# Kernel optimization log

Measured on AMD Instinct MI355X. Metric: run time of the kernel, lower is better.

The kernel has to match this reference:

```python
import jax, jax.numpy as jnp
import numpy as np

ALPHA = 0.2  # LeakyReLU negative slope
NEG_BIG = -9e15

def setup_inputs() -> dict:
    key = jax.random.key(0)
    k1, k2, k3, k4 = jax.random.split(key, 4)
    N, F_in, F_out = 8192, 512, 64
    inp = jax.random.normal(k1, (N, F_in), dtype=jnp.float32)
    adj = jax.random.randint(k2, (N, N), 0, 2, dtype=jnp.int32)
    W = jax.random.normal(k3, (F_in, F_out), dtype=jnp.float32) * (1.414 / np.sqrt(F_in + F_out))
    a = jax.random.normal(k4, (2 * F_out, 1), dtype=jnp.float32) * 0.1
    return {"input": inp, "adj": adj, "W": W, "a": a}

def reference(input, adj, W, a):
    # h: [N, F_out]
    h = input @ W
    F_out = h.shape[1]
    # Decompose a into a1 (source part) and a2 (target part):
    a1 = a[:F_out, 0]   # [F_out]
    a2 = a[F_out:, 0]   # [F_out]
    s1 = h @ a1         # [N]
    s2 = h @ a2         # [N]
    e = s1[:, None] + s2[None, :]                      # [N, N]
    e = jnp.where(e > 0, e, ALPHA * e)                 # LeakyReLU
    e = jnp.where(adj > 0, e, jnp.float32(NEG_BIG))    # mask non-edges
    attention = jax.nn.softmax(e, axis=1)              # [N, N]
    # dropout with p=0.0 / eval mode -> identity
    h_prime = attention @ h                            # [N, F_out]
    return h_prime
```

## Files before the change

kernel.cpp:

```cpp
#include <hip/hip_runtime.h>
#include <hip/hip_bf16.h>

constexpr int N    = 8192;
constexpr int FIN  = 512;
constexpr int FOUT = 64;
constexpr int NSPLIT = 32;
constexpr int JCHUNK = N / NSPLIT;
constexpr int LROW   = JCHUNK + 8;

typedef __attribute__((ext_vector_type(8))) short short8;
typedef __attribute__((ext_vector_type(4))) float f32x4;

__global__ __launch_bounds__(256) void k1_proj(
    const float* __restrict__ input, const float* __restrict__ W,
    const float* __restrict__ a, __hip_bfloat16* __restrict__ hbT,
    float* __restrict__ E1, float* __restrict__ F1,
    float* __restrict__ E2, float* __restrict__ F2)
{
    __shared__ __hip_bfloat16 tile[8][64];
    const int tid  = threadIdx.x;
    const int col  = tid & 63;
    const int g    = tid >> 6;
    const int rbase = blockIdx.x * 8;

    float acc[2] = {0.f, 0.f};
    const float* in0 = input + (size_t)(rbase + g * 2) * FIN;

    for (int k = 0; k < FIN; k += 8) {
        float w[8];
        #pragma unroll
        for (int q = 0; q < 8; ++q) w[q] = W[(k + q) * FOUT + col];
        const float4 x0a = *(const float4*)(in0 + 0 * FIN + k);
        const float4 x0b = *(const float4*)(in0 + 0 * FIN + k + 4);
        const float4 x1a = *(const float4*)(in0 + 1 * FIN + k);
        const float4 x1b = *(const float4*)(in0 + 1 * FIN + k + 4);
        acc[0] = fmaf(x0a.w, w[3], fmaf(x0a.z, w[2], fmaf(x0a.y, w[1], fmaf(x0a.x, w[0], acc[0]))));
        acc[0] = fmaf(x0b.w, w[7], fmaf(x0b.z, w[6], fmaf(x0b.y, w[5], fmaf(x0b.x, w[4], acc[0]))));
        acc[1] = fmaf(x1a.w, w[3], fmaf(x1a.z, w[2], fmaf(x1a.y, w[1], fmaf(x1a.x, w[0], acc[1]))));
        acc[1] = fmaf(x1b.w, w[7], fmaf(x1b.z, w[6], fmaf(x1b.y, w[5], fmaf(x1b.x, w[4], acc[1]))));
    }

    const float a1c = a[col];
    const float a2c = a[FOUT + col];
    #pragma unroll
    for (int q = 0; q < 2; ++q) {
        float r1 = acc[q] * a1c;
        float r2 = acc[q] * a2c;
        #pragma unroll
        for (int off = 32; off >= 1; off >>= 1) {
            r1 += __shfl_xor(r1, off, 64);
            r2 += __shfl_xor(r2, off, 64);
        }
        if (col == 0) {
            const int i = rbase + g * 2 + q;
            E1[i] = __expf(r1);
            F1[i] = __expf(0.2f * r1);
            E2[i] = __expf(r2);
            F2[i] = __expf(0.2f * r2);
        }
        tile[g * 2 + q][col] = __float2bfloat16(acc[q]);
    }
    __syncthreads();

    if (tid < 128) {
        const int c = tid >> 1, part = tid & 1;
        unsigned short v[4];
        #pragma unroll
        for (int u = 0; u < 4; ++u) {
            __hip_bfloat16 hv = tile[part * 4 + u][c];
            v[u] = *reinterpret_cast<unsigned short*>(&hv);
        }
        *(ushort4*)((unsigned short*)hbT + (size_t)c * N + rbase + part * 4) =
            make_ushort4(v[0], v[1], v[2], v[3]);
    }
}

__global__ __launch_bounds__(256, 4) void k2_attn(
    const int* __restrict__ adj,
    const float* __restrict__ E1, const float* __restrict__ F1,
    const float* __restrict__ E2, const float* __restrict__ F2,
    const unsigned short* __restrict__ hbT,
    float* __restrict__ pAcc, float* __restrict__ pZ)
{
    __shared__ unsigned short Bl[64 * LROW];
    __shared__ unsigned int   Ml[64 * 9];
    __shared__ float          E2l[JCHUNK];
    __shared__ float          F2l[JCHUNK];

    const int r   = blockIdx.x;
    const int s   = blockIdx.y;
    const int tid = threadIdx.x;
    const int w     = tid >> 6;
    const int lane  = tid & 63;
    const int row16 = lane & 15;
    const int quad  = lane >> 4;
    const int jbeg  = s * JCHUNK;

    #pragma unroll
    for (int rr = 0; rr < 8; ++rr) {
        const int seg = rr * 256 + tid;
        const int f = seg >> 5, o = seg & 31;
        const short8 v = *(const short8*)((const short*)hbT + (size_t)f * N + jbeg + o * 8);
        *(short8*)(&Bl[f * LROW + o * 8]) = v;
    }
    {
        unsigned char* Mlb = (unsigned char*)Ml;
        #pragma unroll
        for (int it = 0; it < 16; ++it) {
            const int rloc = it * 4 + w;
            const int4 av = *(const int4*)(adj + (size_t)(r * 64 + rloc) * N + jbeg + lane * 4);
            unsigned int nib =
                (av.x != 0 ? 1u : 0u) | (av.y != 0 ? 2u : 0u) |
                (av.z != 0 ? 4u : 0u) | (av.w != 0 ? 8u : 0u);
            const unsigned int other = __shfl_xor(nib, 1, 64);
            if (!(lane & 1))
                Mlb[rloc * 36 + (lane >> 1)] = (unsigned char)(nib | (other << 4));
        }
    }
    E2l[tid] = E2[jbeg + tid];
    F2l[tid] = F2[jbeg + tid];
    __syncthreads();

    const int iloc = w * 16 + row16;
    const int i    = r * 64 + iloc;
    const float E1i = E1[i];
    const float F1i = F1[i];

    f32x4 acc0 = {0.f, 0.f, 0.f, 0.f};
    f32x4 acc1 = {0.f, 0.f, 0.f, 0.f};
    f32x4 acc2 = {0.f, 0.f, 0.f, 0.f};
    f32x4 acc3 = {0.f, 0.f, 0.f, 0.f};
    float zpart = 0.f;

    #pragma unroll
    for (int it = 0; it < JCHUNK / 32; ++it) {
        const int jj = it * 32 + quad * 8;

        const unsigned int mword = Ml[iloc * 9 + it];
        const unsigned int mbyte = (mword >> (8 * quad)) & 0xffu;

        const float4 eA = *(const float4*)(&E2l[jj]);
        const float4 eB = *(const float4*)(&E2l[jj + 4]);
        const float4 fA = *(const float4*)(&F2l[jj]);
        const float4 fB = *(const float4*)(&F2l[jj + 4]);

        const short8 b0 = *(const short8*)(&Bl[(row16 +  0) * LROW + jj]);
        const short8 b1 = *(const short8*)(&Bl[(row16 + 16) * LROW + jj]);
        const short8 b2 = *(const short8*)(&Bl[(row16 + 32) * LROW + jj]);
        const short8 b3 = *(const short8*)(&Bl[(row16 + 48) * LROW + jj]);

        float e2v[8], f2v[8];
        e2v[0] = eA.x; e2v[1] = eA.y; e2v[2] = eA.z; e2v[3] = eA.w;
        e2v[4] = eB.x; e2v[5] = eB.y; e2v[6] = eB.z; e2v[7] = eB.w;
        f2v[0] = fA.x; f2v[1] = fA.y; f2v[2] = fA.z; f2v[3] = fA.w;
        f2v[4] = fB.x; f2v[5] = fB.y; f2v[6] = fB.z; f2v[7] = fB.w;

        short8 afrag;
        #pragma unroll
        for (int j = 0; j < 8; ++j) {
            float pv = fmaxf(E1i * e2v[j], F1i * f2v[j]);
            pv = ((mbyte >> j) & 1u) ? pv : 0.f;
            __hip_bfloat16 hv = __float2bfloat16(pv);
            zpart += __bfloat162float(hv);
            afrag[j] = *reinterpret_cast<short*>(&hv);
        }

        acc0 = __builtin_amdgcn_mfma_f32_16x16x32_bf16(afrag, b0, acc0, 0, 0, 0);
        acc1 = __builtin_amdgcn_mfma_f32_16x16x32_bf16(afrag, b1, acc1, 0, 0, 0);
        acc2 = __builtin_amdgcn_mfma_f32_16x16x32_bf16(afrag, b2, acc2, 0, 0, 0);
        acc3 = __builtin_amdgcn_mfma_f32_16x16x32_bf16(afrag, b3, acc3, 0, 0, 0);
    }

    zpart += __shfl_xor(zpart, 16, 64);
    zpart += __shfl_xor(zpart, 32, 64);
    if (quad == 0) pZ[(size_t)s * N + i] = zpart;

    float* outp = pAcc + ((size_t)s * N + (size_t)r * 64 + w * 16) * FOUT;
    #pragma unroll
    for (int reg = 0; reg < 4; ++reg) {
        const int row = quad * 4 + reg;
        outp[row * FOUT + ( 0 + row16)] = acc0[reg];
        outp[row * FOUT + (16 + row16)] = acc1[reg];
        outp[row * FOUT + (32 + row16)] = acc2[reg];
        outp[row * FOUT + (48 + row16)] = acc3[reg];
    }
}

__global__ __launch_bounds__(256) void k3_combine(
    const float* __restrict__ pAcc, const float* __restrict__ pZ,
    float* __restrict__ out)
{
    const int idx = blockIdx.x * 256 + threadIdx.x;
    const int i = idx >> 6;
    float num = 0.f, den = 0.f;
    #pragma unroll
    for (int s = 0; s < NSPLIT; ++s) {
        num += pAcc[(size_t)s * N * FOUT + idx];
        den += pZ[(size_t)s * N + i];
    }
    out[idx] = num / den;
}

extern "C" void kernel_launch(void* const* d_in, const int* in_sizes, int n_in,
                              void* d_out, int out_size, void* d_ws, size_t ws_size,
                              hipStream_t stream)
{
    const float* input = (const float*)d_in[0];
    const int*   adj   = (const int*)d_in[1];
    const float* W     = (const float*)d_in[2];
    const float* a     = (const float*)d_in[3];
    float* out = (float*)d_out;

    char* ws = (char*)d_ws;
    __hip_bfloat16* hbT = (__hip_bfloat16*)ws;
    float* E1   = (float*)(ws + (size_t)FOUT * N * 2);
    float* F1   = E1 + N;
    float* E2   = F1 + N;
    float* F2   = E2 + N;
    float* pZ   = F2 + N;
    float* pAcc = pZ + (size_t)NSPLIT * N;

    k1_proj<<<N / 8, 256, 0, stream>>>(input, W, a, hbT, E1, F1, E2, F2);

    dim3 g2(N / 64, NSPLIT);
    k2_attn<<<g2, 256, 0, stream>>>(adj, E1, F1, E2, F2,
                                    (const unsigned short*)hbT, pAcc, pZ);

    k3_combine<<<(N * FOUT) / 256, 256, 0, stream>>>(pAcc, pZ, out);
}
```

Measured before the change: 451.9 us.

## Reduce split-K partials by looping slices per block and compute row sums via MFMA

Lowers the number of j-splits from 32 to 8. Each block now walks four 256-column slices of its chunk in sequence, so the pAcc/pZ partial buffers and the combine kernel read a quarter of the data. The row-sum denominator is now computed by an extra MFMA against a ones vector instead of scalar adds plus shuffles. It also uses a packed bf16x2 conversion. In exchange the grid is 4x smaller (1024 blocks), and each slice's loads are serialized behind barriers with no overlap.

```diff
diff --git a/kernel.cpp b/kernel.cpp
--- a/kernel.cpp
+++ b/kernel.cpp
@@ -4,12 +4,16 @@
 constexpr int N    = 8192;
 constexpr int FIN  = 512;
 constexpr int FOUT = 64;
-constexpr int NSPLIT = 32;
+constexpr int NSPLIT = 8;
 constexpr int JCHUNK = N / NSPLIT;
-constexpr int LROW   = JCHUNK + 8;
+constexpr int NSLICE = 4;
+constexpr int JS     = JCHUNK / NSLICE;
+constexpr int LROW   = JS + 8;
 
 typedef __attribute__((ext_vector_type(8))) short short8;
 typedef __attribute__((ext_vector_type(4))) float f32x4;
+
+union BF2U { unsigned int u; __hip_bfloat162 h; };
 
 __global__ __launch_bounds__(256) void k1_proj(
     const float* __restrict__ input, const float* __restrict__ W,
@@ -84,8 +88,8 @@
 {
     __shared__ unsigned short Bl[64 * LROW];
     __shared__ unsigned int   Ml[64 * 9];
-    __shared__ float          E2l[JCHUNK];
-    __shared__ float          F2l[JCHUNK];
+    __shared__ float          E2l[JS];
+    __shared__ float          F2l[JS];
 
     const int r   = blockIdx.x;
     const int s   = blockIdx.y;
@@ -94,86 +98,103 @@
     const int lane  = tid & 63;
     const int row16 = lane & 15;
     const int quad  = lane >> 4;
-    const int jbeg  = s * JCHUNK;
-
-    #pragma unroll
-    for (int rr = 0; rr < 8; ++rr) {
-        const int seg = rr * 256 + tid;
-        const int f = seg >> 5, o = seg & 31;
-        const short8 v = *(const short8*)((const short*)hbT + (size_t)f * N + jbeg + o * 8);
-        *(short8*)(&Bl[f * LROW + o * 8]) = v;
-    }
-    {
-        unsigned char* Mlb = (unsigned char*)Ml;
-        #pragma unroll
-        for (int it = 0; it < 16; ++it) {
-            const int rloc = it * 4 + w;
-            const int4 av = *(const int4*)(adj + (size_t)(r * 64 + rloc) * N + jbeg + lane * 4);
-            unsigned int nib =
-                (av.x != 0 ? 1u : 0u) | (av.y != 0 ? 2u : 0u) |
-                (av.z != 0 ? 4u : 0u) | (av.w != 0 ? 8u : 0u);
-            const unsigned int other = __shfl_xor(nib, 1, 64);
-            if (!(lane & 1))
-                Mlb[rloc * 36 + (lane >> 1)] = (unsigned char)(nib | (other << 4));
-        }
-    }
-    E2l[tid] = E2[jbeg + tid];
-    F2l[tid] = F2[jbeg + tid];
-    __syncthreads();
 
     const int iloc = w * 16 + row16;
     const int i    = r * 64 + iloc;
     const float E1i = E1[i];
     const float F1i = F1[i];
 
+    short8 ones;
+    #pragma unroll
+    for (int q = 0; q < 8; ++q) ones[q] = (short)0x3F80;
+
     f32x4 acc0 = {0.f, 0.f, 0.f, 0.f};
     f32x4 acc1 = {0.f, 0.f, 0.f, 0.f};
     f32x4 acc2 = {0.f, 0.f, 0.f, 0.f};
     f32x4 acc3 = {0.f, 0.f, 0.f, 0.f};
-    float zpart = 0.f;
-
-    #pragma unroll
-    for (int it = 0; it < JCHUNK / 32; ++it) {
-        const int jj = it * 32 + quad * 8;
-
-        const unsigned int mword = Ml[iloc * 9 + it];
-        const unsigned int mbyte = (mword >> (8 * quad)) & 0xffu;
-
-        const float4 eA = *(const float4*)(&E2l[jj]);
-        const float4 eB = *(const float4*)(&E2l[jj + 4]);
-        const float4 fA = *(const float4*)(&F2l[jj]);
-        const float4 fB = *(const float4*)(&F2l[jj + 4]);
-
-        const short8 b0 = *(const short8*)(&Bl[(row16 +  0) * LROW + jj]);
-        const short8 b1 = *(const short8*)(&Bl[(row16 + 16) * LROW + jj]);
-        const short8 b2 = *(const short8*)(&Bl[(row16 + 32) * LROW + jj]);
-        const short8 b3 = *(const short8*)(&Bl[(row16 + 48) * LROW + jj]);
-
-        float e2v[8], f2v[8];
-        e2v[0] = eA.x; e2v[1] = eA.y; e2v[2] = eA.z; e2v[3] = eA.w;
-        e2v[4] = eB.x; e2v[5] = eB.y; e2v[6] = eB.z; e2v[7] = eB.w;
-        f2v[0] = fA.x; f2v[1] = fA.y; f2v[2] = fA.z; f2v[3] = fA.w;
-        f2v[4] = fB.x; f2v[5] = fB.y; f2v[6] = fB.z; f2v[7] = fB.w;
-
-        short8 afrag;
-        #pragma unroll
-        for (int j = 0; j < 8; ++j) {
-            float pv = fmaxf(E1i * e2v[j], F1i * f2v[j]);
-            pv = ((mbyte >> j) & 1u) ? pv : 0.f;
-            __hip_bfloat16 hv = __float2bfloat16(pv);
-            zpart += __bfloat162float(hv);
-            afrag[j] = *reinterpret_cast<short*>(&hv);
-        }
-
-        acc0 = __builtin_amdgcn_mfma_f32_16x16x32_bf16(afrag, b0, acc0, 0, 0, 0);
-        acc1 = __builtin_amdgcn_mfma_f32_16x16x32_bf16(afrag, b1, acc1, 0, 0, 0);
-        acc2 = __builtin_amdgcn_mfma_f32_16x16x32_bf16(afrag, b2, acc2, 0, 0, 0);
-        acc3 = __builtin_amdgcn_mfma_f32_16x16x32_bf16(afrag, b3, acc3, 0, 0, 0);
-    }
-
-    zpart += __shfl_xor(zpart, 16, 64);
-    zpart += __shfl_xor(zpart, 32, 64);
-    if (quad == 0) pZ[(size_t)s * N + i] = zpart;
+    f32x4 accz = {0.f, 0.f, 0.f, 0.f};
+
+    for (int sl = 0; sl < NSLICE; ++sl) {
+        const int jbeg = s * JCHUNK + sl * JS;
+
+        #pragma unroll
+        for (int rr = 0; rr < 8; ++rr) {
+            const int seg = rr * 256 + tid;
+            const int f = seg >> 5, o = seg & 31;
+            const short8 v = *(const short8*)((const short*)hbT + (size_t)f * N + jbeg + o * 8);
+            *(short8*)(&Bl[f * LROW + o * 8]) = v;
+        }
+        {
+            unsigned char* Mlb = (unsigned char*)Ml;
+            #pragma unroll
+            for (int it = 0; it < 16; ++it) {
+                const int rloc = it * 4 + w;
+                const int4 av = *(const int4*)(adj + (size_t)(r * 64 + rloc) * N + jbeg + lane * 4);
+                unsigned int nib =
+                    (av.x != 0 ? 1u : 0u) | (av.y != 0 ? 2u : 0u) |
+                    (av.z != 0 ? 4u : 0u) | (av.w != 0 ? 8u : 0u);
+                const unsigned int other = __shfl_xor(nib, 1, 64);
+                if (!(lane & 1))
+                    Mlb[rloc * 36 + (lane >> 1)] = (unsigned char)(nib | (other << 4));
+            }
+        }
+        E2l[tid] = E2[jbeg + tid];
+        F2l[tid] = F2[jbeg + tid];
+        __syncthreads();
+
+        #pragma unroll
+        for (int it = 0; it < JS / 32; ++it) {
+            const int jj = it * 32 + quad * 8;
+
+            const unsigned int mword = Ml[iloc * 9 + it];
+            const unsigned int mbyte = (mword >> (8 * quad)) & 0xffu;
+
+            const float4 eA = *(const float4*)(&E2l[jj]);
+            const float4 eB = *(const float4*)(&E2l[jj + 4]);
+            const float4 fA = *(const float4*)(&F2l[jj]);
+            const float4 fB = *(const float4*)(&F2l[jj + 4]);
+
+            const short8 b0 = *(const short8*)(&Bl[(row16 +  0) * LROW + jj]);
+            const short8 b1 = *(const short8*)(&Bl[(row16 + 16) * LROW + jj]);
+            const short8 b2 = *(const short8*)(&Bl[(row16 + 32) * LROW + jj]);
+            const short8 b3 = *(const short8*)(&Bl[(row16 + 48) * LROW + jj]);
+
+            float e2v[8], f2v[8];
+            e2v[0] = eA.x; e2v[1] = eA.y; e2v[2] = eA.z; e2v[3] = eA.w;
+            e2v[4] = eB.x; e2v[5] = eB.y; e2v[6] = eB.z; e2v[7] = eB.w;
+            f2v[0] = fA.x; f2v[1] = fA.y; f2v[2] = fA.z; f2v[3] = fA.w;
+            f2v[4] = fB.x; f2v[5] = fB.y; f2v[6] = fB.z; f2v[7] = fB.w;
+
+            float pv[8];
+            #pragma unroll
+            for (int j = 0; j < 8; ++j) {
+                float p = fmaxf(E1i * e2v[j], F1i * f2v[j]);
+                pv[j] = ((mbyte >> j) & 1u) ? p : 0.f;
+            }
+
+            short8 afrag;
+            #pragma unroll
+            for (int jp = 0; jp < 4; ++jp) {
+                BF2U cv;
+                cv.h = __float22bfloat162_rn(make_float2(pv[2 * jp], pv[2 * jp + 1]));
+                afrag[2 * jp]     = (short)(cv.u & 0xffffu);
+                afrag[2 * jp + 1] = (short)(cv.u >> 16);
+            }
+
+            acc0 = __builtin_amdgcn_mfma_f32_16x16x32_bf16(afrag, b0, acc0, 0, 0, 0);
+            acc1 = __builtin_amdgcn_mfma_f32_16x16x32_bf16(afrag, b1, acc1, 0, 0, 0);
+            acc2 = __builtin_amdgcn_mfma_f32_16x16x32_bf16(afrag, b2, acc2, 0, 0, 0);
+            acc3 = __builtin_amdgcn_mfma_f32_16x16x32_bf16(afrag, b3, acc3, 0, 0, 0);
+            accz = __builtin_amdgcn_mfma_f32_16x16x32_bf16(afrag, ones, accz, 0, 0, 0);
+        }
+        __syncthreads();
+    }
+
+    if (row16 == 0) {
+        #pragma unroll
+        for (int reg = 0; reg < 4; ++reg)
+            pZ[(size_t)s * N + r * 64 + w * 16 + quad * 4 + reg] = accz[reg];
+    }
 
     float* outp = pAcc + ((size_t)s * N + (size_t)r * 64 + w * 16) * FOUT;
     #pragma unroll
```

New measurement: 439.6 us. 1.03x faster.
